# Optimization experiments

Measured on AMD Instinct MI355X. Metric: run time of the kernel, lower is better.

Reference implementation:

```python
import jax, jax.numpy as jnp
import numpy as np

B, N, D = 2, 256, 512
H = 4 * D  # mlp_hidden_dim


def setup_inputs() -> dict:
    key = jax.random.key(0)
    ks = jax.random.split(key, 14)
    s_in = 1.0 / np.sqrt(D)
    s_h = 1.0 / np.sqrt(H)
    s_cat = 1.0 / np.sqrt(2 * D)
    return {
        "x_v": jax.random.normal(ks[0], (B, N, D), jnp.float32),
        "x_a": jax.random.normal(ks[1], (B, N, D), jnp.float32),
        # weights stored as (in, out); y = x @ W + b (same math as torch Linear)
        "W1v": jax.random.uniform(ks[2], (D, H), jnp.float32, -s_in, s_in),
        "b1v": jax.random.uniform(ks[3], (H,), jnp.float32, -s_in, s_in),
        "W1a": jax.random.uniform(ks[4], (D, H), jnp.float32, -s_in, s_in),
        "b1a": jax.random.uniform(ks[5], (H,), jnp.float32, -s_in, s_in),
        "Wmv": jax.random.uniform(ks[6], (H, D), jnp.float32, -s_h, s_h),
        "bmv": jax.random.uniform(ks[7], (D,), jnp.float32, -s_h, s_h),
        "Wma": jax.random.uniform(ks[8], (H, D), jnp.float32, -s_h, s_h),
        "bma": jax.random.uniform(ks[9], (D,), jnp.float32, -s_h, s_h),
        "Wout": jax.random.uniform(ks[10], (2 * D, D), jnp.float32, -s_cat, s_cat),
        "bout": jax.random.uniform(ks[11], (D,), jnp.float32, -s_cat, s_cat),
    }


def reference(x_v, x_a, W1v, b1v, W1a, b1a, Wmv, bmv, Wma, bma, Wout, bout):
    # pairwise Manhattan distance: [B, N, M]
    dist = jnp.sum(jnp.abs(x_v[:, :, None, :] - x_a[:, None, :, :]), axis=-1)
    dv = dist.mean(axis=2)  # [B, N] mean distance of each v-token to all a-tokens
    da = dist.mean(axis=1)  # [B, M]
    xv_w = x_v * dv[..., None]
    xa_w = x_a * da[..., None]
    # dropout prob = 0.0 -> identity
    hv = jax.nn.gelu(xv_w @ W1v + b1v, approximate=False) @ Wmv + bmv
    ha = jax.nn.gelu(xa_w @ W1a + b1a, approximate=False) @ Wma + bma
    combined = jnp.concatenate([hv, ha], axis=-1)  # [B, N, 2D]
    return combined @ Wout + bout
```

## Files before the change

### kernel.cpp

```cpp
#include <hip/hip_runtime.h>
#include <math.h>

#define Bsz  2
#define Ntok 256
#define Ddim 512
#define Hdim 2048
#define Mrows 512

typedef __bf16 bf16_8 __attribute__((ext_vector_type(8)));
typedef __bf16 bf16_4 __attribute__((ext_vector_type(4)));
typedef float  f32x4_t __attribute__((ext_vector_type(4)));

struct PrepPtrs {
    const float* src[5];
    __bf16*      dst[5];
    const float* xv;
    const float* xa;
    float*       pv;
    float*       pa;
    float*       out;
};

__global__ __launch_bounds__(256) void prep_kernel(PrepPtrs p) {
    __shared__ float tile[32][33];
    __shared__ float red[4][4];

    int blk = blockIdx.x;
    int tid = threadIdx.x;

    if (blk < 4608) {
        const int Ks[5]  = {512, 512, 2048, 2048, 1024};
        const int Ns[5]  = {2048, 2048, 512, 512, 512};
        const int off[6] = {0, 1024, 2048, 3072, 4096, 4608};
        int mi = 0;
        while (blk >= off[mi + 1]) ++mi;
        int local = blk - off[mi];
        int shift = (mi < 2) ? 6 : 4;
        int bx = local & ((1 << shift) - 1);
        int by = local >> shift;
        const float* src = p.src[mi];
        __bf16*      dst = p.dst[mi];
        int K = Ks[mi], N = Ns[mi];
        int n0 = bx << 5, k0 = by << 5;

        int kl = tid >> 3, nl = (tid & 7) << 2;
        float4 v = *(const float4*)&src[(size_t)(k0 + kl) * N + n0 + nl];
        tile[kl][nl + 0] = v.x;
        tile[kl][nl + 1] = v.y;
        tile[kl][nl + 2] = v.z;
        tile[kl][nl + 3] = v.w;
        __syncthreads();
        int nl2 = tid >> 3, kl2 = (tid & 7) << 2;
        bf16_4 o;
#pragma unroll
        for (int i = 0; i < 4; ++i) o[i] = (__bf16)tile[kl2 + i][nl2];
        *(bf16_4*)&dst[(size_t)(n0 + nl2) * K + k0 + kl2] = o;
    } else if (blk < 5632) {
        int bx   = blk - 4608;
        int jc   = bx & 3;
        int g    = bx >> 2;
        int role = g >> 7;
        int b    = (g >> 6) & 1;
        int i0   = (g & 63) << 2;
        const float* Q    = role ? p.xa : p.xv;
        const float* S    = role ? p.xv : p.xa;
        float*       outp = role ? p.pa : p.pv;

        int d0 = tid << 1;
        const float* Qb = Q + ((size_t)b * Ntok + i0) * Ddim + d0;
        const float* Sb = S + ((size_t)b * Ntok + (jc << 6)) * Ddim + d0;

        float2 q[4];
#pragma unroll
        for (int r = 0; r < 4; ++r) q[r] = *(const float2*)(Qb + r * Ddim);

        float acc[4] = {0.f, 0.f, 0.f, 0.f};
#pragma unroll 4
        for (int j = 0; j < 64; ++j) {
            float2 s = *(const float2*)(Sb + (size_t)j * Ddim);
#pragma unroll
            for (int r = 0; r < 4; ++r)
                acc[r] += fabsf(q[r].x - s.x) + fabsf(q[r].y - s.y);
        }
        int lane = tid & 63, wv = tid >> 6;
#pragma unroll
        for (int r = 0; r < 4; ++r) {
            float v = acc[r];
#pragma unroll
            for (int off2 = 32; off2; off2 >>= 1) v += __shfl_down(v, off2);
            if (lane == 0) red[wv][r] = v;
        }
        __syncthreads();
        if (tid < 4) {
            float v = red[0][tid] + red[1][tid] + red[2][tid] + red[3][tid];
            outp[jc * Mrows + b * Ntok + i0 + tid] = v;
        }
    } else {
        int zb = blk - 5632;
        float4 z4 = {0.f, 0.f, 0.f, 0.f};
        *(float4*)&p.out[((size_t)zb * 256 + tid) * 4] = z4;
    }
}

template <int GELU, int AMODE, int OUTM>
__device__ void gemm_tile(__bf16 (&As)[2][64][40], __bf16 (&Bs)[2][64][40],
                          const void* Aa, const void* Ab, int lda,
                          const __bf16* BT, int ldb,
                          const float* bias, const float* scale4,
                          void* C, int ldc, int Kdim,
                          int m0, int n0, int addBias) {
    const int tid = threadIdx.x;
    const int row = tid >> 2;
    const int kc  = (tid & 3) << 3;

    const __bf16* Bp  = BT + (size_t)(n0 + row) * ldb + kc;
    const float*  Af0 = nullptr;
    const float*  Af1 = nullptr;
    const __bf16* Abp = nullptr;
    float s = 1.0f;
    if (AMODE == 1) {
        Af0 = (const float*)Aa + (size_t)(m0 + row) * lda + kc;
        int m = m0 + row;
        s = (scale4[m] + scale4[Mrows + m] + scale4[2 * Mrows + m] +
             scale4[3 * Mrows + m]) * (1.0f / 256.0f);
    } else if (AMODE == 2) {
        Af0 = (const float*)Aa + (size_t)(m0 + row) * lda + kc;
        Af1 = (const float*)Ab + (size_t)(m0 + row) * lda + kc;
    } else {
        Abp = (const __bf16*)Aa + (size_t)(m0 + row) * lda + kc;
    }

    const int wave = tid >> 6, lane = tid & 63;
    const int moff = (wave >> 1) << 5, noff = (wave & 1) << 5;
    const int lrow = lane & 15, quad = lane >> 4;

    float4 rA0, rA1, rB0, rB1, nA0, nA1, nB0, nB1;
    bf16_8 ra8, na8;
    bf16_8 rb8, nb8;

    auto loadStage = [&](int kt, float4& fa0, float4& fa1, float4& fb0,
                         float4& fb1, bf16_8& a8, bf16_8& b8) {
        b8 = *(const bf16_8*)(Bp + kt);
        if (AMODE == 0) {
            a8 = *(const bf16_8*)(Abp + kt);
        } else {
            fa0 = *(const float4*)(Af0 + kt);
            fa1 = *(const float4*)(Af0 + kt + 4);
            if (AMODE == 2) {
                fb0 = *(const float4*)(Af1 + kt);
                fb1 = *(const float4*)(Af1 + kt + 4);
            }
        }
    };
    auto storeStage = [&](int buf, const float4& fa0, const float4& fa1,
                          const float4& fb0, const float4& fb1,
                          const bf16_8& a8in, const bf16_8& b8in) {
        bf16_8 a8;
        if (AMODE == 0) {
            a8 = a8in;
        } else if (AMODE == 1) {
            a8[0] = (__bf16)(fa0.x * s); a8[1] = (__bf16)(fa0.y * s);
            a8[2] = (__bf16)(fa0.z * s); a8[3] = (__bf16)(fa0.w * s);
            a8[4] = (__bf16)(fa1.x * s); a8[5] = (__bf16)(fa1.y * s);
            a8[6] = (__bf16)(fa1.z * s); a8[7] = (__bf16)(fa1.w * s);
        } else {
            a8[0] = (__bf16)(fa0.x + fb0.x); a8[1] = (__bf16)(fa0.y + fb0.y);
            a8[2] = (__bf16)(fa0.z + fb0.z); a8[3] = (__bf16)(fa0.w + fb0.w);
            a8[4] = (__bf16)(fa1.x + fb1.x); a8[5] = (__bf16)(fa1.y + fb1.y);
            a8[6] = (__bf16)(fa1.z + fb1.z); a8[7] = (__bf16)(fa1.w + fb1.w);
        }
        *(bf16_8*)&As[buf][row][kc] = a8;
        *(bf16_8*)&Bs[buf][row][kc] = b8in;
    };

    f32x4_t acc00 = {0.f, 0.f, 0.f, 0.f};
    f32x4_t acc01 = {0.f, 0.f, 0.f, 0.f};
    f32x4_t acc10 = {0.f, 0.f, 0.f, 0.f};
    f32x4_t acc11 = {0.f, 0.f, 0.f, 0.f};

    const int nIter = Kdim >> 5;

    loadStage(0, rA0, rA1, rB0, rB1, ra8, rb8);
    storeStage(0, rA0, rA1, rB0, rB1, ra8, rb8);
    if (nIter > 1) loadStage(32, rA0, rA1, rB0, rB1, ra8, rb8);
    __syncthreads();

    for (int it = 0; it < nIter; ++it) {
        const int cur = it & 1;
        bf16_8 a0 = *(const bf16_8*)&As[cur][moff + lrow][quad << 3];
        bf16_8 a1 = *(const bf16_8*)&As[cur][moff + 16 + lrow][quad << 3];
        bf16_8 b0 = *(const bf16_8*)&Bs[cur][noff + lrow][quad << 3];
        bf16_8 b1 = *(const bf16_8*)&Bs[cur][noff + 16 + lrow][quad << 3];
        if (it + 2 < nIter)
            loadStage((it + 2) << 5, nA0, nA1, nB0, nB1, na8, nb8);
        acc00 = __builtin_amdgcn_mfma_f32_16x16x32_bf16(a0, b0, acc00, 0, 0, 0);
        acc01 = __builtin_amdgcn_mfma_f32_16x16x32_bf16(a0, b1, acc01, 0, 0, 0);
        acc10 = __builtin_amdgcn_mfma_f32_16x16x32_bf16(a1, b0, acc10, 0, 0, 0);
        acc11 = __builtin_amdgcn_mfma_f32_16x16x32_bf16(a1, b1, acc11, 0, 0, 0);
        if (it + 1 < nIter) {
            storeStage(cur ^ 1, rA0, rA1, rB0, rB1, ra8, rb8);
            rA0 = nA0; rA1 = nA1; rB0 = nB0; rB1 = nB1; ra8 = na8; rb8 = nb8;
            __syncthreads();
        }
    }

    f32x4_t accs[2][2] = {{acc00, acc01}, {acc10, acc11}};
#pragma unroll
    for (int ti = 0; ti < 2; ++ti) {
#pragma unroll
        for (int tj = 0; tj < 2; ++tj) {
            int colg = n0 + noff + (tj << 4) + lrow;
            float bv = addBias ? bias[colg] : 0.0f;
#pragma unroll
            for (int r = 0; r < 4; ++r) {
                int rowg = m0 + moff + (ti << 4) + (quad << 2) + r;
                float v = accs[ti][tj][r] + bv;
                if (GELU) v = 0.5f * v * (1.0f + erff(v * 0.70710678118654752f));
                if (OUTM == 1)
                    ((__bf16*)C)[(size_t)rowg * ldc + colg] = (__bf16)v;
                else if (OUTM == 0)
                    ((float*)C)[(size_t)rowg * ldc + colg] = v;
                else
                    atomicAdd((float*)C + (size_t)rowg * ldc + colg, v);
            }
        }
    }
}

struct FPtrs {
    const float*  x[2];
    const __bf16* WT1[2];
    const float*  b1[2];
    const float*  pd[2];
    __bf16*       g1[2];
    const __bf16* WTm[2];
    const float*  bm[2];
    float*        part[2];
    const __bf16* WTout;
    const float*  bout;
    float*        out;
};

__global__ __launch_bounds__(256) void gemm1_kernel(FPtrs p) {
    __shared__ __align__(16) __bf16 As[2][64][40];
    __shared__ __align__(16) __bf16 Bs[2][64][40];
    int z = blockIdx.z;
    gemm_tile<1, 1, 1>(As, Bs, p.x[z], nullptr, Ddim, p.WT1[z], Ddim,
                       p.b1[z], p.pd[z], p.g1[z], Hdim, Ddim,
                       blockIdx.y << 6, blockIdx.x << 6, 1);
}

__global__ __launch_bounds__(256) void gemm2_kernel(FPtrs p) {
    __shared__ __align__(16) __bf16 As[2][64][40];
    __shared__ __align__(16) __bf16 Bs[2][64][40];
    int zz = blockIdx.z, z = zz & 1, kz = zz >> 1;
    gemm_tile<0, 0, 0>(As, Bs, p.g1[z] + kz * 1024, nullptr, Hdim,
                       p.WTm[z] + kz * 1024, Hdim, p.bm[z], nullptr,
                       p.part[kz] + z * Ddim, 2 * Ddim, 1024,
                       blockIdx.y << 6, blockIdx.x << 6, kz == 0);
}

__global__ __launch_bounds__(256) void gemm3_kernel(FPtrs p) {
    __shared__ __align__(16) __bf16 As[2][64][40];
    __shared__ __align__(16) __bf16 Bs[2][64][40];
    int kz = blockIdx.z;
    gemm_tile<0, 2, 2>(As, Bs, p.part[0] + kz * 256, p.part[1] + kz * 256,
                       2 * Ddim, p.WTout + kz * 256, 2 * Ddim, p.bout,
                       nullptr, p.out, Ddim, 256,
                       blockIdx.y << 6, blockIdx.x << 6, kz == 0);
}

extern "C" void kernel_launch(void* const* d_in, const int* in_sizes, int n_in,
                              void* d_out, int out_size, void* d_ws, size_t ws_size,
                              hipStream_t stream) {
    const float* x_v  = (const float*)d_in[0];
    const float* x_a  = (const float*)d_in[1];
    const float* W1v  = (const float*)d_in[2];
    const float* b1v  = (const float*)d_in[3];
    const float* W1a  = (const float*)d_in[4];
    const float* b1a  = (const float*)d_in[5];
    const float* Wmv  = (const float*)d_in[6];
    const float* bmv  = (const float*)d_in[7];
    const float* Wma  = (const float*)d_in[8];
    const float* bma  = (const float*)d_in[9];
    const float* Wout = (const float*)d_in[10];
    const float* bout = (const float*)d_in[11];
    float* out = (float*)d_out;

    char* w = (char*)d_ws;
    auto alloc = [&](size_t bytes) {
        char* r = w;
        w += (bytes + 255) & ~(size_t)255;
        return (void*)r;
    };
    float*    pv    = (float*)alloc(4 * Mrows * 4);
    float*    pa    = (float*)alloc(4 * Mrows * 4);
    __bf16*   WT1v  = (__bf16*)alloc((size_t)Hdim * Ddim * 2);
    __bf16*   WT1a  = (__bf16*)alloc((size_t)Hdim * Ddim * 2);
    __bf16*   WTmv  = (__bf16*)alloc((size_t)Ddim * Hdim * 2);
    __bf16*   WTma  = (__bf16*)alloc((size_t)Ddim * Hdim * 2);
    __bf16*   WTout = (__bf16*)alloc((size_t)Ddim * 2 * Ddim * 2);
    __bf16*   g1v   = (__bf16*)alloc((size_t)Mrows * Hdim * 2);
    __bf16*   g1a   = (__bf16*)alloc((size_t)Mrows * Hdim * 2);
    float*    part0 = (float*)alloc((size_t)Mrows * 2 * Ddim * 4);
    float*    part1 = (float*)alloc((size_t)Mrows * 2 * Ddim * 4);

    PrepPtrs pp;
    pp.src[0] = W1v;  pp.dst[0] = WT1v;
    pp.src[1] = W1a;  pp.dst[1] = WT1a;
    pp.src[2] = Wmv;  pp.dst[2] = WTmv;
    pp.src[3] = Wma;  pp.dst[3] = WTma;
    pp.src[4] = Wout; pp.dst[4] = WTout;
    pp.xv = x_v; pp.xa = x_a; pp.pv = pv; pp.pa = pa;
    pp.out = out;
    prep_kernel<<<dim3(5888), dim3(256), 0, stream>>>(pp);

    FPtrs fp;
    fp.x[0] = x_v; fp.x[1] = x_a;
    fp.WT1[0] = WT1v; fp.WT1[1] = WT1a;
    fp.b1[0] = b1v; fp.b1[1] = b1a;
    fp.pd[0] = pv; fp.pd[1] = pa;
    fp.g1[0] = g1v; fp.g1[1] = g1a;
    fp.WTm[0] = WTmv; fp.WTm[1] = WTma;
    fp.bm[0] = bmv; fp.bm[1] = bma;
    fp.part[0] = part0; fp.part[1] = part1;
    fp.WTout = WTout; fp.bout = bout;
    fp.out = out;

    gemm1_kernel<<<dim3(Hdim / 64, Mrows / 64, 2), dim3(256), 0, stream>>>(fp);
    gemm2_kernel<<<dim3(8, 8, 4), dim3(256), 0, stream>>>(fp);
    gemm3_kernel<<<dim3(8, 8, 4), dim3(256), 0, stream>>>(fp);
}
```

Measured before the change: 135.2 us.

## Fold second MLP and output projections into combined weights, fuse stages

The MLP second-layer weights are pre-multiplied with the matching halves of Wout, giving combined WcT matrices, and the biases are folded into a single combined bias vector. The intermediate hv/ha partial buffers and one GEMM stage go away, as does transposing Wmv/Wma. The first GEMM and the weight-combination GEMMs run concurrently in one launch, followed by a single split-K GEMM into the output. This cuts launches and the round trips of intermediate activations, but it adds an extra bf16 rounding of the combined weights, which can cost accuracy. The transpose tiles are also enlarged to 64x64.

```diff
diff --git a/kernel.cpp b/kernel.cpp
--- a/kernel.cpp
+++ b/kernel.cpp
@@ -12,51 +12,60 @@
 typedef float  f32x4_t __attribute__((ext_vector_type(4)));
 
 struct PrepPtrs {
-    const float* src[5];
-    __bf16*      dst[5];
+    const float* src[3];
+    __bf16*      dst[3];
     const float* xv;
     const float* xa;
     float*       pv;
     float*       pa;
     float*       out;
+    float*       bc;
 };
 
 __global__ __launch_bounds__(256) void prep_kernel(PrepPtrs p) {
-    __shared__ float tile[32][33];
+    __shared__ float tile[64][65];
     __shared__ float red[4][4];
 
     int blk = blockIdx.x;
     int tid = threadIdx.x;
 
-    if (blk < 4608) {
-        const int Ks[5]  = {512, 512, 2048, 2048, 1024};
-        const int Ns[5]  = {2048, 2048, 512, 512, 512};
-        const int off[6] = {0, 1024, 2048, 3072, 4096, 4608};
+    if (blk < 640) {
+        const int Ks[3]  = {512, 512, 1024};
+        const int Ns[3]  = {2048, 2048, 512};
+        const int off[4] = {0, 256, 512, 640};
         int mi = 0;
         while (blk >= off[mi + 1]) ++mi;
         int local = blk - off[mi];
-        int shift = (mi < 2) ? 6 : 4;
+        int shift = (mi < 2) ? 5 : 3;
         int bx = local & ((1 << shift) - 1);
         int by = local >> shift;
         const float* src = p.src[mi];
         __bf16*      dst = p.dst[mi];
         int K = Ks[mi], N = Ns[mi];
-        int n0 = bx << 5, k0 = by << 5;
-
-        int kl = tid >> 3, nl = (tid & 7) << 2;
-        float4 v = *(const float4*)&src[(size_t)(k0 + kl) * N + n0 + nl];
-        tile[kl][nl + 0] = v.x;
-        tile[kl][nl + 1] = v.y;
-        tile[kl][nl + 2] = v.z;
-        tile[kl][nl + 3] = v.w;
+        int n0 = bx << 6, k0 = by << 6;
+
+        int klb = tid >> 4, nl = (tid & 15) << 2;
+#pragma unroll
+        for (int pass = 0; pass < 4; ++pass) {
+            int kl = (pass << 4) + klb;
+            float4 v = *(const float4*)&src[(size_t)(k0 + kl) * N + n0 + nl];
+            tile[kl][nl + 0] = v.x;
+            tile[kl][nl + 1] = v.y;
+            tile[kl][nl + 2] = v.z;
+            tile[kl][nl + 3] = v.w;
+        }
         __syncthreads();
-        int nl2 = tid >> 3, kl2 = (tid & 7) << 2;
-        bf16_4 o;
-#pragma unroll
-        for (int i = 0; i < 4; ++i) o[i] = (__bf16)tile[kl2 + i][nl2];
-        *(bf16_4*)&dst[(size_t)(n0 + nl2) * K + k0 + kl2] = o;
-    } else if (blk < 5632) {
-        int bx   = blk - 4608;
+        int nl2 = tid >> 2, kb = (tid & 3) << 2;
+#pragma unroll
+        for (int pass = 0; pass < 4; ++pass) {
+            int kl2 = (pass << 4) + kb;
+            bf16_4 o;
+#pragma unroll
+            for (int i = 0; i < 4; ++i) o[i] = (__bf16)tile[kl2 + i][nl2];
+            *(bf16_4*)&dst[(size_t)(n0 + nl2) * K + k0 + kl2] = o;
+        }
+    } else if (blk < 1664) {
+        int bx   = blk - 640;
         int jc   = bx & 3;
         int g    = bx >> 2;
         int role = g >> 7;
@@ -96,16 +105,16 @@
             outp[jc * Mrows + b * Ntok + i0 + tid] = v;
         }
     } else {
-        int zb = blk - 5632;
+        int zb = blk - 1664;
         float4 z4 = {0.f, 0.f, 0.f, 0.f};
         *(float4*)&p.out[((size_t)zb * 256 + tid) * 4] = z4;
-    }
-}
-
-template <int GELU, int AMODE, int OUTM>
+        if (zb == 0 && tid < 128) *(float4*)&p.bc[tid * 4] = z4;
+    }
+}
+
+template <int GELU, int AMODE, int BFP32, int OUTM>
 __device__ void gemm_tile(__bf16 (&As)[2][64][40], __bf16 (&Bs)[2][64][40],
-                          const void* Aa, const void* Ab, int lda,
-                          const __bf16* BT, int ldb,
+                          const void* Aa, int lda, const void* Bv, int ldb,
                           const float* bias, const float* scale4,
                           void* C, int ldc, int Kdim,
                           int m0, int n0, int addBias) {
@@ -113,64 +122,61 @@
     const int row = tid >> 2;
     const int kc  = (tid & 3) << 3;
 
-    const __bf16* Bp  = BT + (size_t)(n0 + row) * ldb + kc;
-    const float*  Af0 = nullptr;
-    const float*  Af1 = nullptr;
-    const __bf16* Abp = nullptr;
+    const __bf16* Bb  = (const __bf16*)Bv + (size_t)(n0 + row) * ldb + kc;
+    const float*  Bf  = (const float*)Bv + (size_t)(n0 + row) * ldb + kc;
+    const float*  Af  = (const float*)Aa + (size_t)(m0 + row) * lda + kc;
+    const __bf16* Ab  = (const __bf16*)Aa + (size_t)(m0 + row) * lda + kc;
     float s = 1.0f;
     if (AMODE == 1) {
-        Af0 = (const float*)Aa + (size_t)(m0 + row) * lda + kc;
         int m = m0 + row;
         s = (scale4[m] + scale4[Mrows + m] + scale4[2 * Mrows + m] +
              scale4[3 * Mrows + m]) * (1.0f / 256.0f);
-    } else if (AMODE == 2) {
-        Af0 = (const float*)Aa + (size_t)(m0 + row) * lda + kc;
-        Af1 = (const float*)Ab + (size_t)(m0 + row) * lda + kc;
-    } else {
-        Abp = (const __bf16*)Aa + (size_t)(m0 + row) * lda + kc;
     }
 
     const int wave = tid >> 6, lane = tid & 63;
     const int moff = (wave >> 1) << 5, noff = (wave & 1) << 5;
     const int lrow = lane & 15, quad = lane >> 4;
 
-    float4 rA0, rA1, rB0, rB1, nA0, nA1, nB0, nB1;
-    bf16_8 ra8, na8;
-    bf16_8 rb8, nb8;
-
-    auto loadStage = [&](int kt, float4& fa0, float4& fa1, float4& fb0,
-                         float4& fb1, bf16_8& a8, bf16_8& b8) {
-        b8 = *(const bf16_8*)(Bp + kt);
-        if (AMODE == 0) {
-            a8 = *(const bf16_8*)(Abp + kt);
+    struct Stage {
+        float4 aF0, aF1, bF0, bF1;
+        bf16_8 a8, b8;
+    };
+    Stage sR, sN;
+
+    auto loadStage = [&](int kt, Stage& st) {
+        if (BFP32) {
+            st.bF0 = *(const float4*)(Bf + kt);
+            st.bF1 = *(const float4*)(Bf + kt + 4);
         } else {
-            fa0 = *(const float4*)(Af0 + kt);
-            fa1 = *(const float4*)(Af0 + kt + 4);
-            if (AMODE == 2) {
-                fb0 = *(const float4*)(Af1 + kt);
-                fb1 = *(const float4*)(Af1 + kt + 4);
-            }
+            st.b8 = *(const bf16_8*)(Bb + kt);
+        }
+        if (AMODE == 1) {
+            st.aF0 = *(const float4*)(Af + kt);
+            st.aF1 = *(const float4*)(Af + kt + 4);
+        } else {
+            st.a8 = *(const bf16_8*)(Ab + kt);
         }
     };
-    auto storeStage = [&](int buf, const float4& fa0, const float4& fa1,
-                          const float4& fb0, const float4& fb1,
-                          const bf16_8& a8in, const bf16_8& b8in) {
-        bf16_8 a8;
-        if (AMODE == 0) {
-            a8 = a8in;
-        } else if (AMODE == 1) {
-            a8[0] = (__bf16)(fa0.x * s); a8[1] = (__bf16)(fa0.y * s);
-            a8[2] = (__bf16)(fa0.z * s); a8[3] = (__bf16)(fa0.w * s);
-            a8[4] = (__bf16)(fa1.x * s); a8[5] = (__bf16)(fa1.y * s);
-            a8[6] = (__bf16)(fa1.z * s); a8[7] = (__bf16)(fa1.w * s);
+    auto storeStage = [&](int buf, const Stage& st) {
+        bf16_8 a8, b8;
+        if (AMODE == 1) {
+            a8[0] = (__bf16)(st.aF0.x * s); a8[1] = (__bf16)(st.aF0.y * s);
+            a8[2] = (__bf16)(st.aF0.z * s); a8[3] = (__bf16)(st.aF0.w * s);
+            a8[4] = (__bf16)(st.aF1.x * s); a8[5] = (__bf16)(st.aF1.y * s);
+            a8[6] = (__bf16)(st.aF1.z * s); a8[7] = (__bf16)(st.aF1.w * s);
         } else {
-            a8[0] = (__bf16)(fa0.x + fb0.x); a8[1] = (__bf16)(fa0.y + fb0.y);
-            a8[2] = (__bf16)(fa0.z + fb0.z); a8[3] = (__bf16)(fa0.w + fb0.w);
-            a8[4] = (__bf16)(fa1.x + fb1.x); a8[5] = (__bf16)(fa1.y + fb1.y);
-            a8[6] = (__bf16)(fa1.z + fb1.z); a8[7] = (__bf16)(fa1.w + fb1.w);
+            a8 = st.a8;
+        }
+        if (BFP32) {
+            b8[0] = (__bf16)st.bF0.x; b8[1] = (__bf16)st.bF0.y;
+            b8[2] = (__bf16)st.bF0.z; b8[3] = (__bf16)st.bF0.w;
+            b8[4] = (__bf16)st.bF1.x; b8[5] = (__bf16)st.bF1.y;
+            b8[6] = (__bf16)st.bF1.z; b8[7] = (__bf16)st.bF1.w;
+        } else {
+            b8 = st.b8;
         }
         *(bf16_8*)&As[buf][row][kc] = a8;
-        *(bf16_8*)&Bs[buf][row][kc] = b8in;
+        *(bf16_8*)&Bs[buf][row][kc] = b8;
     };
 
     f32x4_t acc00 = {0.f, 0.f, 0.f, 0.f};
@@ -180,9 +186,9 @@
 
     const int nIter = Kdim >> 5;
 
-    loadStage(0, rA0, rA1, rB0, rB1, ra8, rb8);
-    storeStage(0, rA0, rA1, rB0, rB1, ra8, rb8);
-    if (nIter > 1) loadStage(32, rA0, rA1, rB0, rB1, ra8, rb8);
+    loadStage(0, sR);
+    storeStage(0, sR);
+    if (nIter > 1) loadStage(32, sR);
     __syncthreads();
 
     for (int it = 0; it < nIter; ++it) {
@@ -191,15 +197,14 @@
         bf16_8 a1 = *(const bf16_8*)&As[cur][moff + 16 + lrow][quad << 3];
         bf16_8 b0 = *(const bf16_8*)&Bs[cur][noff + lrow][quad << 3];
         bf16_8 b1 = *(const bf16_8*)&Bs[cur][noff + 16 + lrow][quad << 3];
-        if (it + 2 < nIter)
-            loadStage((it + 2) << 5, nA0, nA1, nB0, nB1, na8, nb8);
+        if (it + 2 < nIter) loadStage((it + 2) << 5, sN);
         acc00 = __builtin_amdgcn_mfma_f32_16x16x32_bf16(a0, b0, acc00, 0, 0, 0);
         acc01 = __builtin_amdgcn_mfma_f32_16x16x32_bf16(a0, b1, acc01, 0, 0, 0);
         acc10 = __builtin_amdgcn_mfma_f32_16x16x32_bf16(a1, b0, acc10, 0, 0, 0);
         acc11 = __builtin_amdgcn_mfma_f32_16x16x32_bf16(a1, b1, acc11, 0, 0, 0);
         if (it + 1 < nIter) {
-            storeStage(cur ^ 1, rA0, rA1, rB0, rB1, ra8, rb8);
-            rA0 = nA0; rA1 = nA1; rB0 = nB0; rB1 = nB1; ra8 = na8; rb8 = nb8;
+            storeStage(cur ^ 1, sR);
+            sR = sN;
             __syncthreads();
         }
     }
@@ -218,8 +223,6 @@
                 if (GELU) v = 0.5f * v * (1.0f + erff(v * 0.70710678118654752f));
                 if (OUTM == 1)
                     ((__bf16*)C)[(size_t)rowg * ldc + colg] = (__bf16)v;
-                else if (OUTM == 0)
-                    ((float*)C)[(size_t)rowg * ldc + colg] = v;
                 else
                     atomicAdd((float*)C + (size_t)rowg * ldc + colg, v);
             }
@@ -227,47 +230,73 @@
     }
 }
 
-struct FPtrs {
+struct APtrs {
     const float*  x[2];
     const __bf16* WT1[2];
     const float*  b1[2];
     const float*  pd[2];
     __bf16*       g1[2];
-    const __bf16* WTm[2];
+    const __bf16* WTout;
+    const float*  Wm[2];
     const float*  bm[2];
-    float*        part[2];
-    const __bf16* WTout;
+    const float*  Wout;
     const float*  bout;
+    __bf16*       WcT[2];
+    float*        bc;
+};
+
+__global__ __launch_bounds__(256) void kernelA(APtrs p) {
+    __shared__ __align__(16) __bf16 As[2][64][40];
+    __shared__ __align__(16) __bf16 Bs[2][64][40];
+    int blk = blockIdx.x;
+    if (blk < 512) {
+        int z = blk >> 8, t = blk & 255;
+        int mt = t >> 5, nt = t & 31;
+        gemm_tile<1, 1, 0, 1>(As, Bs, p.x[z], Ddim, p.WT1[z], Ddim,
+                              p.b1[z], p.pd[z], p.g1[z], Hdim, Ddim,
+                              mt << 6, nt << 6, 1);
+    } else if (blk < 1024) {
+        int b2 = blk - 512;
+        int z = b2 >> 8, t = b2 & 255;
+        int mt = t >> 5, nt = t & 31;
+        gemm_tile<0, 0, 1, 1>(As, Bs, p.WTout + z * 512, 2 * Ddim,
+                              p.Wm[z], Ddim, nullptr, nullptr,
+                              p.WcT[z], Hdim, Ddim, mt << 6, nt << 6, 0);
+    } else {
+        int kb = blk - 1024;
+        int tid = threadIdx.x;
+        float a0 = 0.f, a1 = 0.f, a2 = 0.f, a3 = 0.f;
+#pragma unroll 4
+        for (int kk = 0; kk < 128; kk += 2) {
+            int k0 = (kb << 7) + kk, k1 = k0 + 1;
+            float bk0 = (k0 < 512) ? p.bm[0][k0] : p.bm[1][k0 - 512];
+            float bk1 = (k1 < 512) ? p.bm[0][k1] : p.bm[1][k1 - 512];
+            a0 += bk0 * p.Wout[(size_t)k0 * Ddim + tid];
+            a1 += bk0 * p.Wout[(size_t)k0 * Ddim + tid + 256];
+            a2 += bk1 * p.Wout[(size_t)k1 * Ddim + tid];
+            a3 += bk1 * p.Wout[(size_t)k1 * Ddim + tid + 256];
+        }
+        if (kb == 0) { a0 += p.bout[tid]; a1 += p.bout[tid + 256]; }
+        atomicAdd(&p.bc[tid],       a0 + a2);
+        atomicAdd(&p.bc[tid + 256], a1 + a3);
+    }
+}
+
+struct BPtrs {
+    const __bf16* g1[2];
+    const __bf16* WcT[2];
+    const float*  bc;
     float*        out;
 };
 
-__global__ __launch_bounds__(256) void gemm1_kernel(FPtrs p) {
+__global__ __launch_bounds__(256) void kernelB(BPtrs p) {
     __shared__ __align__(16) __bf16 As[2][64][40];
     __shared__ __align__(16) __bf16 Bs[2][64][40];
-    int z = blockIdx.z;
-    gemm_tile<1, 1, 1>(As, Bs, p.x[z], nullptr, Ddim, p.WT1[z], Ddim,
-                       p.b1[z], p.pd[z], p.g1[z], Hdim, Ddim,
-                       blockIdx.y << 6, blockIdx.x << 6, 1);
-}
-
-__global__ __launch_bounds__(256) void gemm2_kernel(FPtrs p) {
-    __shared__ __align__(16) __bf16 As[2][64][40];
-    __shared__ __align__(16) __bf16 Bs[2][64][40];
-    int zz = blockIdx.z, z = zz & 1, kz = zz >> 1;
-    gemm_tile<0, 0, 0>(As, Bs, p.g1[z] + kz * 1024, nullptr, Hdim,
-                       p.WTm[z] + kz * 1024, Hdim, p.bm[z], nullptr,
-                       p.part[kz] + z * Ddim, 2 * Ddim, 1024,
-                       blockIdx.y << 6, blockIdx.x << 6, kz == 0);
-}
-
-__global__ __launch_bounds__(256) void gemm3_kernel(FPtrs p) {
-    __shared__ __align__(16) __bf16 As[2][64][40];
-    __shared__ __align__(16) __bf16 Bs[2][64][40];
-    int kz = blockIdx.z;
-    gemm_tile<0, 2, 2>(As, Bs, p.part[0] + kz * 256, p.part[1] + kz * 256,
-                       2 * Ddim, p.WTout + kz * 256, 2 * Ddim, p.bout,
-                       nullptr, p.out, Ddim, 256,
-                       blockIdx.y << 6, blockIdx.x << 6, kz == 0);
+    int nt = blockIdx.x & 7, mt = (blockIdx.x >> 3) & 7, kz = blockIdx.x >> 6;
+    int z = kz >> 2, koff = (kz & 3) << 9;
+    gemm_tile<0, 0, 0, 2>(As, Bs, p.g1[z] + koff, Hdim, p.WcT[z] + koff, Hdim,
+                          p.bc, nullptr, p.out, Ddim, Ddim,
+                          mt << 6, nt << 6, kz == 0);
 }
 
 extern "C" void kernel_launch(void* const* d_in, const int* in_sizes, int n_in,
@@ -295,39 +324,40 @@
     };
     float*    pv    = (float*)alloc(4 * Mrows * 4);
     float*    pa    = (float*)alloc(4 * Mrows * 4);
+    float*    bc    = (float*)alloc(Ddim * 4);
     __bf16*   WT1v  = (__bf16*)alloc((size_t)Hdim * Ddim * 2);
     __bf16*   WT1a  = (__bf16*)alloc((size_t)Hdim * Ddim * 2);
-    __bf16*   WTmv  = (__bf16*)alloc((size_t)Ddim * Hdim * 2);
-    __bf16*   WTma  = (__bf16*)alloc((size_t)Ddim * Hdim * 2);
     __bf16*   WTout = (__bf16*)alloc((size_t)Ddim * 2 * Ddim * 2);
+    __bf16*   WcTv  = (__bf16*)alloc((size_t)Ddim * Hdim * 2);
+    __bf16*   WcTa  = (__bf16*)alloc((size_t)Ddim * Hdim * 2);
     __bf16*   g1v   = (__bf16*)alloc((size_t)Mrows * Hdim * 2);
     __bf16*   g1a   = (__bf16*)alloc((size_t)Mrows * Hdim * 2);
-    float*    part0 = (float*)alloc((size_t)Mrows * 2 * Ddim * 4);
-    float*    part1 = (float*)alloc((size_t)Mrows * 2 * Ddim * 4);
 
     PrepPtrs pp;
     pp.src[0] = W1v;  pp.dst[0] = WT1v;
     pp.src[1] = W1a;  pp.dst[1] = WT1a;
-    pp.src[2] = Wmv;  pp.dst[2] = WTmv;
-    pp.src[3] = Wma;  pp.dst[3] = WTma;
-    pp.src[4] = Wout; pp.dst[4] = WTout;
+    pp.src[2] = Wout; pp.dst[2] = WTout;
     pp.xv = x_v; pp.xa = x_a; pp.pv = pv; pp.pa = pa;
-    pp.out = out;
-    prep_kernel<<<dim3(5888), dim3(256), 0, stream>>>(pp);
-
-    FPtrs fp;
-    fp.x[0] = x_v; fp.x[1] = x_a;
-    fp.WT1[0] = WT1v; fp.WT1[1] = WT1a;
-    fp.b1[0] = b1v; fp.b1[1] = b1a;
-    fp.pd[0] = pv; fp.pd[1] = pa;
-    fp.g1[0] = g1v; fp.g1[1] = g1a;
-    fp.WTm[0] = WTmv; fp.WTm[1] = WTma;
-    fp.bm[0] = bmv; fp.bm[1] = bma;
-    fp.part[0] = part0; fp.part[1] = part1;
-    fp.WTout = WTout; fp.bout = bout;
-    fp.out = out;
-
-    gemm1_kernel<<<dim3(Hdim / 64, Mrows / 64, 2), dim3(256), 0, stream>>>(fp);
-    gemm2_kernel<<<dim3(8, 8, 4), dim3(256), 0, stream>>>(fp);
-    gemm3_kernel<<<dim3(8, 8, 4), dim3(256), 0, stream>>>(fp);
-}
+    pp.out = out; pp.bc = bc;
+    prep_kernel<<<dim3(1920), dim3(256), 0, stream>>>(pp);
+
+    APtrs ap;
+    ap.x[0] = x_v; ap.x[1] = x_a;
+    ap.WT1[0] = WT1v; ap.WT1[1] = WT1a;
+    ap.b1[0] = b1v; ap.b1[1] = b1a;
+    ap.pd[0] = pv; ap.pd[1] = pa;
+    ap.g1[0] = g1v; ap.g1[1] = g1a;
+    ap.WTout = WTout;
+    ap.Wm[0] = Wmv; ap.Wm[1] = Wma;
+    ap.bm[0] = bmv; ap.bm[1] = bma;
+    ap.Wout = Wout; ap.bout = bout;
+    ap.WcT[0] = WcTv; ap.WcT[1] = WcTa;
+    ap.bc = bc;
+    kernelA<<<dim3(1032), dim3(256), 0, stream>>>(ap);
+
+    BPtrs bp;
+    bp.g1[0] = g1v; bp.g1[1] = g1a;
+    bp.WcT[0] = WcTv; bp.WcT[1] = WcTa;
+    bp.bc = bc; bp.out = out;
+    kernelB<<<dim3(512), dim3(256), 0, stream>>>(bp);
+}
```

New measurement: 130.6 us. -3.4%, faster.
